# Optimization experiments

Measured on AMD Instinct MI355X. Metric: run time of the kernel, lower is better.

## Reference

```python
import jax, jax.numpy as jnp
import numpy as np

N, E, F_IN, HID, H, NG = 50000, 800000, 128, 64, 3, 50

def gatv2_layer(x, src, dst, Wsrc, bsrc, Wdst, bdst, attn, n_nodes):
    # DGL GATv2Conv: e_ij = attn . leaky_relu(Wsrc x_j + Wdst x_i), softmax over dst, aggregate Wsrc x_j
    Hh, O = attn.shape
    fs = (x @ Wsrc + bsrc).reshape(-1, Hh, O)  # [N,H,O]
    fd = (x @ Wdst + bdst).reshape(-1, Hh, O)
    e = jax.nn.leaky_relu(fs[src] + fd[dst], 0.2)          # [E,H,O]
    logits = jnp.einsum('eho,ho->eh', e, attn)             # [E,H]
    m = jax.ops.segment_max(logits, dst, num_segments=n_nodes)
    m = jnp.where(jnp.isfinite(m), m, 0.0)
    ex = jnp.exp(logits - m[dst])
    den = jax.ops.segment_sum(ex, dst, num_segments=n_nodes)
    alpha = ex / jnp.maximum(den[dst], 1e-9)               # edge softmax
    return jax.ops.segment_sum(alpha[..., None] * fs[src], dst, num_segments=n_nodes)  # [N,H,O]

def setup_inputs() -> dict:
    key = jax.random.key(0)
    ks = jax.random.split(key, 32)
    d = {}
    d['x'] = jax.random.normal(ks[0], (N, F_IN), jnp.float32)
    d['src'] = jax.random.randint(ks[1], (E,), 0, N)
    d['dst'] = jax.random.randint(ks[2], (E,), 0, N)
    d['graph_ids'] = jnp.sort(jax.random.randint(ks[3], (N,), 0, NG))
    d['n_graphs'] = NG
    ins = [F_IN, HID * H, HID * H]
    i = 4
    for l, fin in enumerate(ins, 1):
        s = 1.0 / np.sqrt(fin)
        d[f'Wsrc{l}'] = jax.random.normal(ks[i], (fin, H * HID), jnp.float32) * s; i += 1
        d[f'bsrc{l}'] = jnp.zeros((H * HID,), jnp.float32)
        d[f'Wdst{l}'] = jax.random.normal(ks[i], (fin, H * HID), jnp.float32) * s; i += 1
        d[f'bdst{l}'] = jnp.zeros((H * HID,), jnp.float32)
        d[f'attn{l}'] = jax.random.normal(ks[i], (H, HID), jnp.float32) * s; i += 1
    for name, (a, b) in [('1', (HID, 64)), ('2', (64, 32)), ('3', (32, 2))]:
        s = 1.0 / np.sqrt(a)
        d[f'W{name}'] = jax.random.normal(ks[i], (a, b), jnp.float32) * s; i += 1
        d[f'b{name}'] = jnp.zeros((b,), jnp.float32)
    return d

def forward(x, src, dst, graph_ids, n_graphs,
            Wsrc1, bsrc1, Wdst1, bdst1, attn1,
            Wsrc2, bsrc2, Wdst2, bdst2, attn2,
            Wsrc3, bsrc3, Wdst3, bdst3, attn3,
            W1, b1, W2, b2, W3, b3):
    n = x.shape[0]
    h = gatv2_layer(x, src, dst, Wsrc1, bsrc1, Wdst1, bdst1, attn1, n).reshape(n, -1)
    h = gatv2_layer(h, src, dst, Wsrc2, bsrc2, Wdst2, bdst2, attn2, n).reshape(n, -1)
    h = gatv2_layer(h, src, dst, Wsrc3, bsrc3, Wdst3, bdst3, attn3, n).mean(axis=1)  # [N,HID]
    # dgl.mean_nodes: per-graph mean pooling
    sums = jax.ops.segment_sum(h, graph_ids, num_segments=n_graphs)
    cnts = jax.ops.segment_sum(jnp.ones((n,), h.dtype), graph_ids, num_segments=n_graphs)
    g = sums / jnp.maximum(cnts, 1.0)[:, None]  # [NG,HID]
    lrelu = lambda t: jax.nn.leaky_relu(t, 0.01)
    out = lrelu(g @ W1 + b1)
    out = lrelu(out @ W2 + b2)
    out = lrelu(out @ W3 + b3)
    return out

def reference(x, src, dst, graph_ids, n_graphs,
              Wsrc1, bsrc1, Wdst1, bdst1, attn1,
              Wsrc2, bsrc2, Wdst2, bdst2, attn2,
              Wsrc3, bsrc3, Wdst3, bdst3, attn3,
              W1, b1, W2, b2, W3, b3):
    return forward(x, src, dst, graph_ids, n_graphs,
                   Wsrc1, bsrc1, Wdst1, bdst1, attn1,
                   Wsrc2, bsrc2, Wdst2, bdst2, attn2,
                   Wsrc3, bsrc3, Wdst3, bdst3, attn3,
                   W1, b1, W2, b2, W3, b3)
```

## Files before the change

kernel.cpp:

```cpp
#include <hip/hip_runtime.h>
#include <math.h>

#define N_NODES 50000
#define N_EDGES 800000
#define F_INPUT 128
#define HID 64
#define NHEAD 3
#define NGRAPH 50
#define D1 192
#define D2 384
#define NF 24
#define MF 3125

typedef __attribute__((ext_vector_type(8))) short bf16x8;
typedef __attribute__((ext_vector_type(4))) short short4v;
typedef __attribute__((ext_vector_type(4))) float f32x4;

#define ROR_ADD(v, C) \
  ((v) + __int_as_float(__builtin_amdgcn_update_dpp(0, __float_as_int(v), (C), 0xF, 0xF, true)))

__device__ __forceinline__ unsigned short f2bf(float x) {
  unsigned u = __float_as_uint(x);
  return (unsigned short)((u + 0x7FFFu + ((u >> 16) & 1u)) >> 16);
}
__device__ __forceinline__ float bf2f(unsigned short h) {
  return __uint_as_float(((unsigned)h) << 16);
}
__device__ __forceinline__ void split3(float x, unsigned short& o1, unsigned short& o2, unsigned short& o3) {
  o1 = f2bf(x); float f1 = bf2f(o1);
  float r1 = x - f1; o2 = f2bf(r1); float f2 = bf2f(o2);
  o3 = f2bf(r1 - f2);
}


__global__ void zero_int_kernel(int* __restrict__ p, int n) {
  int i = blockIdx.x * blockDim.x + threadIdx.x;
  if (i < n) p[i] = 0;
}

__global__ void hist_kernel(const int* __restrict__ dst, int* __restrict__ counts, int e) {
  int i = blockIdx.x * blockDim.x + threadIdx.x;
  if (i < e) atomicAdd(&counts[dst[i]], 1);
}

__global__ __launch_bounds__(256)
void scan_blocks_kernel(const int* __restrict__ counts, int* __restrict__ indptr,
                        int* __restrict__ bsum, int n) {
  __shared__ int wt[4];
  int tid = threadIdx.x, lane = tid & 63, wid = tid >> 6;
  int i = blockIdx.x * 256 + tid;
  int x = (i < n) ? counts[i] : 0;
  #pragma unroll
  for (int off = 1; off < 64; off <<= 1) {
    int t = __shfl_up(x, off, 64);
    if (lane >= off) x += t;
  }
  if (lane == 63) wt[wid] = x;
  __syncthreads();
  int woff = 0;
  #pragma unroll
  for (int w = 0; w < 4; ++w) if (w < wid) woff += wt[w];
  x += woff;
  if (i < n) indptr[i + 1] = x;
  if (tid == 255) bsum[blockIdx.x] = x;
}

__global__ __launch_bounds__(256)
void scan_sums_kernel(int* __restrict__ bsum, int nb) {
  __shared__ int wt[4];
  int tid = threadIdx.x, lane = tid & 63, wid = tid >> 6;
  int v = (tid < nb) ? bsum[tid] : 0;
  int x = v;
  #pragma unroll
  for (int off = 1; off < 64; off <<= 1) {
    int t = __shfl_up(x, off, 64);
    if (lane >= off) x += t;
  }
  if (lane == 63) wt[wid] = x;
  __syncthreads();
  int woff = 0;
  #pragma unroll
  for (int w = 0; w < 4; ++w) if (w < wid) woff += wt[w];
  if (tid < nb) bsum[tid] = woff + x - v;
}

__global__ void add_offs_kernel(int* __restrict__ indptr, const int* __restrict__ bsum,
                                int* __restrict__ cursor, int n) {
  int i = blockIdx.x * 256 + threadIdx.x;
  if (i == 0) { indptr[0] = 0; cursor[0] = 0; }
  if (i < n) {
    int v = indptr[i + 1] + bsum[blockIdx.x];
    indptr[i + 1] = v;
    if (i + 1 < n) cursor[i + 1] = v;
  }
}

__global__ void scatter_kernel(const int* __restrict__ src, const int* __restrict__ dst,
                               int* __restrict__ cursor, int* __restrict__ ssrc, int e) {
  int i = blockIdx.x * blockDim.x + threadIdx.x;
  if (i < e) {
    int pos = atomicAdd(&cursor[dst[i]], 1);
    ssrc[pos] = src[i];
  }
}


__global__ __launch_bounds__(256)
void wconv_kernel(const float* __restrict__ Wsrc, const float* __restrict__ Wdst,
                  const float* __restrict__ bsrc, const float* __restrict__ bdst,
                  int K, unsigned short* __restrict__ wfrag, float* __restrict__ biasf) {
  int t = blockIdx.x * 256 + threadIdx.x;
  if (t < D2) biasf[t] = (t < D1) ? bsrc[t] : bdst[t - D1];
  int KS = K >> 5;
  int total = KS * NF * 3 * 64;
  if (t >= total) return;
  int lane = t & 63;
  int q = t >> 6;
  int pl = q % 3; q /= 3;
  int nf = q % NF;
  int ks = q / NF;
  int n = nf * 16 + (lane & 15);
  int kg = lane >> 4;
  unsigned short out[8];
  #pragma unroll
  for (int j = 0; j < 8; ++j) {
    int k = ks * 32 + kg * 4 + (j & 3) + ((j >> 2) << 4);
    float w = (n < D1) ? Wsrc[(size_t)k * D1 + n] : Wdst[(size_t)k * D1 + (n - D1)];
    unsigned short s1, s2, s3;
    split3(w, s1, s2, s3);
    out[j] = (pl == 0) ? s1 : (pl == 1) ? s2 : s3;
  }
  *(bf16x8*)(wfrag + (size_t)t * 8) = *(bf16x8*)out;
}


__global__ __launch_bounds__(256)
void aconv_kernel(const float* __restrict__ A, unsigned short* __restrict__ P,
                  int n4, size_t MK) {
  int t = blockIdx.x * 256 + threadIdx.x;
  if (t >= n4) return;
  float4 v = ((const float4*)A)[t];
  unsigned short s1[4], s2[4], s3[4];
  split3(v.x, s1[0], s2[0], s3[0]);
  split3(v.y, s1[1], s2[1], s3[1]);
  split3(v.z, s1[2], s2[2], s3[2]);
  split3(v.w, s1[3], s2[3], s3[3]);
  ((short4v*)P)[t]        = *(short4v*)s1;
  ((short4v*)(P + MK))[t] = *(short4v*)s2;
  ((short4v*)(P + 2 * MK))[t] = *(short4v*)s3;
}


__global__ __launch_bounds__(256, 2)
void mfma_gemm_kernel(const unsigned short* __restrict__ Ap,
                      const unsigned short* __restrict__ Wf,
                      const float* __restrict__ biasf,
                      int K, float* __restrict__ C) {
  __shared__ unsigned short Bs[NF * 3 * 64 * 8];
  const int tid = threadIdx.x;
  const int lane = tid & 63, wid = tid >> 6;
  const int mf = blockIdx.x * 4 + wid;
  const bool active = (mf < MF);
  const int rowl = lane & 15;
  const int kg = lane >> 4;
  const size_t MK = (size_t)N_NODES * K;
  const int KS = K >> 5;

  f32x4 acc[NF];
  #pragma unroll
  for (int nf = 0; nf < NF; ++nf) acc[nf] = (f32x4){0.f, 0.f, 0.f, 0.f};

  const size_t arow = (size_t)(mf * 16 + rowl) * K;

  for (int ks = 0; ks < KS; ++ks) {
    {
      const float4* s = (const float4*)(Wf + (size_t)ks * (NF * 3 * 64 * 8));
      float4* d = (float4*)Bs;
      #pragma unroll
      for (int i = 0; i < 18; ++i) d[tid + i * 256] = s[tid + i * 256];
    }
    __syncthreads();
    if (active) {
      union { bf16x8 v; short4v h[2]; } ua1, ua2, ua3;
      const unsigned short* a0 = Ap + arow + ks * 32 + kg * 4;
      ua1.h[0] = *(const short4v*)(a0);
      ua1.h[1] = *(const short4v*)(a0 + 16);
      ua2.h[0] = *(const short4v*)(a0 + MK);
      ua2.h[1] = *(const short4v*)(a0 + MK + 16);
      ua3.h[0] = *(const short4v*)(a0 + 2 * MK);
      ua3.h[1] = *(const short4v*)(a0 + 2 * MK + 16);
      bf16x8 a1 = ua1.v, a2 = ua2.v, a3 = ua3.v;
      #pragma unroll
      for (int nf = 0; nf < NF; ++nf) {
        bf16x8 b1 = *(const bf16x8*)&Bs[(nf * 3 + 0) * 512 + lane * 8];
        bf16x8 b2 = *(const bf16x8*)&Bs[(nf * 3 + 1) * 512 + lane * 8];
        bf16x8 b3 = *(const bf16x8*)&Bs[(nf * 3 + 2) * 512 + lane * 8];
        acc[nf] = __builtin_amdgcn_mfma_f32_16x16x32_bf16(a1, b1, acc[nf], 0, 0, 0);
        acc[nf] = __builtin_amdgcn_mfma_f32_16x16x32_bf16(a1, b2, acc[nf], 0, 0, 0);
        acc[nf] = __builtin_amdgcn_mfma_f32_16x16x32_bf16(a2, b1, acc[nf], 0, 0, 0);
        acc[nf] = __builtin_amdgcn_mfma_f32_16x16x32_bf16(a1, b3, acc[nf], 0, 0, 0);
        acc[nf] = __builtin_amdgcn_mfma_f32_16x16x32_bf16(a2, b2, acc[nf], 0, 0, 0);
        acc[nf] = __builtin_amdgcn_mfma_f32_16x16x32_bf16(a3, b1, acc[nf], 0, 0, 0);
      }
    }
    __syncthreads();
  }

  if (active) {
    const int rowb = mf * 16 + kg * 4;
    #pragma unroll
    for (int nf = 0; nf < NF; ++nf) {
      int col = nf * 16 + rowl;
      float bb = biasf[col];
      float* cp = C + (size_t)rowb * D2 + col;
      cp[0]        = acc[nf][0] + bb;
      cp[D2]       = acc[nf][1] + bb;
      cp[2 * D2]   = acc[nf][2] + bb;
      cp[3 * D2]   = acc[nf][3] + bb;
    }
  }
}


template <int LAST>
__global__ __launch_bounds__(256)
void edge_kernel(const float* __restrict__ fsfd, const int* __restrict__ indptr,
                 const int* __restrict__ ssrc, const float* __restrict__ attn,
                 void* __restrict__ outv) {
  int wave = (blockIdx.x * blockDim.x + threadIdx.x) >> 6;
  if (wave >= N_NODES) return;
  int lane = threadIdx.x & 63;
  int grp = lane >> 4;
  int l16 = lane & 15;
  int db = l16 * 4;
  const int node = wave;
  const float LOG2E = 1.4426950408889634f;

  float fd[12], a[12];
  {
    const float* fdp = fsfd + (size_t)node * D2 + D1;
    *(float4*)&fd[0] = *(const float4*)(fdp + db);
    *(float4*)&fd[4] = *(const float4*)(fdp + 64 + db);
    *(float4*)&fd[8] = *(const float4*)(fdp + 128 + db);
    float4 a0 = *(const float4*)(attn + db);
    float4 a1 = *(const float4*)(attn + 64 + db);
    float4 a2 = *(const float4*)(attn + 128 + db);
    a[0]=a0.x*LOG2E; a[1]=a0.y*LOG2E; a[2]=a0.z*LOG2E; a[3]=a0.w*LOG2E;
    a[4]=a1.x*LOG2E; a[5]=a1.y*LOG2E; a[6]=a1.z*LOG2E; a[7]=a1.w*LOG2E;
    a[8]=a2.x*LOG2E; a[9]=a2.y*LOG2E; a[10]=a2.z*LOG2E; a[11]=a2.w*LOG2E;
  }
  int beg = indptr[node], end = indptr[node + 1];
  int deg = end - beg;
  int nit = (deg + 3) >> 2;

  float m[3] = {-INFINITY, -INFINITY, -INFINITY};
  float d[3] = {0.f, 0.f, 0.f};
  float c[12] = {0,0,0,0,0,0,0,0,0,0,0,0};
  float f[12] = {0,0,0,0,0,0,0,0,0,0,0,0};
  float g[12] = {0,0,0,0,0,0,0,0,0,0,0,0};

  int e0 = beg + grp;
  if (e0 < end) {
    int s = ssrc[e0];
    const float* p = fsfd + (size_t)s * D2;
    *(float4*)&f[0] = *(const float4*)(p + db);
    *(float4*)&f[4] = *(const float4*)(p + 64 + db);
    *(float4*)&f[8] = *(const float4*)(p + 128 + db);
  }
  int sNext = 0;
  { int e1 = e0 + 4; if (e1 < end) sNext = ssrc[e1]; }

  for (int it = 0; it < nit; ++it) {
    int eC = e0 + it * 4;
    int eN = eC + 4;
    int sNN = 0;
    { int e2 = eC + 8; if (e2 < end) sNN = ssrc[e2]; }
    if (eN < end) {
      const float* p = fsfd + (size_t)sNext * D2;
      *(float4*)&g[0] = *(const float4*)(p + db);
      *(float4*)&g[4] = *(const float4*)(p + 64 + db);
      *(float4*)&g[8] = *(const float4*)(p + 128 + db);
    }
    float ph0 = 0.f, ph1 = 0.f, ph2 = 0.f;
    #pragma unroll
    for (int i = 0; i < 4; ++i) {
      float t = f[i] + fd[i]; t = fmaxf(t, 0.2f * t); ph0 = fmaf(t, a[i], ph0);
    }
    #pragma unroll
    for (int i = 4; i < 8; ++i) {
      float t = f[i] + fd[i]; t = fmaxf(t, 0.2f * t); ph1 = fmaf(t, a[i], ph1);
    }
    #pragma unroll
    for (int i = 8; i < 12; ++i) {
      float t = f[i] + fd[i]; t = fmaxf(t, 0.2f * t); ph2 = fmaf(t, a[i], ph2);
    }
    ph0 = ROR_ADD(ph0, 0x128); ph1 = ROR_ADD(ph1, 0x128); ph2 = ROR_ADD(ph2, 0x128);
    ph0 = ROR_ADD(ph0, 0x124); ph1 = ROR_ADD(ph1, 0x124); ph2 = ROR_ADD(ph2, 0x124);
    ph0 = ROR_ADD(ph0, 0x122); ph1 = ROR_ADD(ph1, 0x122); ph2 = ROR_ADD(ph2, 0x122);
    ph0 = ROR_ADD(ph0, 0x121); ph1 = ROR_ADD(ph1, 0x121); ph2 = ROR_ADD(ph2, 0x121);
    if (eC < end) {
      {
        float nm = fmaxf(m[0], ph0);
        float ex = exp2f(-fabsf(ph0 - m[0]));
        float sc = (ph0 > m[0]) ? ex : 1.f;
        float p  = (ph0 > m[0]) ? 1.f : ex;
        d[0] = d[0] * sc + p; m[0] = nm;
        #pragma unroll
        for (int j = 0; j < 4; ++j) c[j] = fmaf(p, f[j], c[j] * sc);
      }
      {
        float nm = fmaxf(m[1], ph1);
        float ex = exp2f(-fabsf(ph1 - m[1]));
        float sc = (ph1 > m[1]) ? ex : 1.f;
        float p  = (ph1 > m[1]) ? 1.f : ex;
        d[1] = d[1] * sc + p; m[1] = nm;
        #pragma unroll
        for (int j = 0; j < 4; ++j) c[4 + j] = fmaf(p, f[4 + j], c[4 + j] * sc);
      }
      {
        float nm = fmaxf(m[2], ph2);
        float ex = exp2f(-fabsf(ph2 - m[2]));
        float sc = (ph2 > m[2]) ? ex : 1.f;
        float p  = (ph2 > m[2]) ? 1.f : ex;
        d[2] = d[2] * sc + p; m[2] = nm;
        #pragma unroll
        for (int j = 0; j < 4; ++j) c[8 + j] = fmaf(p, f[8 + j], c[8 + j] * sc);
      }
    }
    #pragma unroll
    for (int i = 0; i < 12; ++i) f[i] = g[i];
    sNext = sNN;
  }

  float M0 = m[0], M1 = m[1], M2 = m[2];
  #pragma unroll
  for (int off = 16; off < 64; off <<= 1) {
    M0 = fmaxf(M0, __shfl_xor(M0, off, 64));
    M1 = fmaxf(M1, __shfl_xor(M1, off, 64));
    M2 = fmaxf(M2, __shfl_xor(M2, off, 64));
  }
  float s0 = (m[0] == M0) ? 1.f : exp2f(m[0] - M0);
  float s1 = (m[1] == M1) ? 1.f : exp2f(m[1] - M1);
  float s2f = (m[2] == M2) ? 1.f : exp2f(m[2] - M2);
  d[0] *= s0; d[1] *= s1; d[2] *= s2f;
  #pragma unroll
  for (int j = 0; j < 4; ++j) { c[j] *= s0; c[4 + j] *= s1; c[8 + j] *= s2f; }
  #pragma unroll
  for (int off = 16; off < 64; off <<= 1) {
    d[0] += __shfl_xor(d[0], off, 64);
    d[1] += __shfl_xor(d[1], off, 64);
    d[2] += __shfl_xor(d[2], off, 64);
    #pragma unroll
    for (int i = 0; i < 12; ++i) c[i] += __shfl_xor(c[i], off, 64);
  }
  float r[12];
  float i0 = d[0] > 0.f ? 1.f / d[0] : 0.f;
  float i1 = d[1] > 0.f ? 1.f / d[1] : 0.f;
  float i2 = d[2] > 0.f ? 1.f / d[2] : 0.f;
  #pragma unroll
  for (int j = 0; j < 4; ++j) { r[j] = c[j] * i0; r[4 + j] = c[4 + j] * i1; r[8 + j] = c[8 + j] * i2; }

  if (grp == 0) {
    if (LAST) {
      float* out = (float*)outv;
      float4 o;
      o.x = (r[0] + r[4] + r[8])  * (1.f / 3.f);
      o.y = (r[1] + r[5] + r[9])  * (1.f / 3.f);
      o.z = (r[2] + r[6] + r[10]) * (1.f / 3.f);
      o.w = (r[3] + r[7] + r[11]) * (1.f / 3.f);
      *(float4*)(out + (size_t)node * HID + db) = o;
    } else {
      unsigned short* P = (unsigned short*)outv;
      const size_t MK2 = (size_t)N_NODES * D1;
      unsigned short s1[12], s2[12], s3[12];
      #pragma unroll
      for (int i = 0; i < 12; ++i) split3(r[i], s1[i], s2[i], s3[i]);
      #pragma unroll
      for (int hh = 0; hh < 3; ++hh) {
        size_t base = (size_t)node * D1 + hh * 64 + db;
        *(short4v*)(P + base)           = *(short4v*)&s1[hh * 4];
        *(short4v*)(P + MK2 + base)     = *(short4v*)&s2[hh * 4];
        *(short4v*)(P + 2 * MK2 + base) = *(short4v*)&s3[hh * 4];
      }
    }
  }
}


__global__ __launch_bounds__(256)
void pool_mlp_kernel(const float* __restrict__ h, const int* __restrict__ gids,
                     const float* __restrict__ W1, const float* __restrict__ b1,
                     const float* __restrict__ W2, const float* __restrict__ b2,
                     const float* __restrict__ W3, const float* __restrict__ b3,
                     float* __restrict__ out) {
  int g = blockIdx.x;
  int tid = threadIdx.x;
  int lane = tid & 63, wid = tid >> 6;
  int lo, hi;
  { int l = 0, r = N_NODES; while (l < r) { int mid = (l + r) >> 1; if (gids[mid] < g) l = mid + 1; else r = mid; } lo = l; }
  { int l = 0, r = N_NODES; while (l < r) { int mid = (l + r) >> 1; if (gids[mid] < g + 1) l = mid + 1; else r = mid; } hi = l; }
  float s = 0.f;
  for (int i = lo + wid; i < hi; i += 4) s += h[(size_t)i * HID + lane];
  __shared__ float red[4][64];
  __shared__ float gv[64], o1[64], o2[32];
  red[wid][lane] = s;
  __syncthreads();
  if (tid < 64) {
    float tot = red[0][tid] + red[1][tid] + red[2][tid] + red[3][tid];
    float cnt = (float)(hi - lo);
    gv[tid] = tot / fmaxf(cnt, 1.f);
  }
  __syncthreads();
  if (tid < 64) {
    float t = b1[tid];
    for (int k = 0; k < 64; ++k) t = fmaf(gv[k], W1[k * 64 + tid], t);
    o1[tid] = t > 0.f ? t : 0.01f * t;
  }
  __syncthreads();
  if (tid < 32) {
    float t = b2[tid];
    for (int k = 0; k < 64; ++k) t = fmaf(o1[k], W2[k * 32 + tid], t);
    o2[tid] = t > 0.f ? t : 0.01f * t;
  }
  __syncthreads();
  if (tid < 2) {
    float t = b3[tid];
    for (int k = 0; k < 32; ++k) t = fmaf(o2[k], W3[k * 2 + tid], t);
    out[g * 2 + tid] = t > 0.f ? t : 0.01f * t;
  }
}


extern "C" void kernel_launch(void* const* d_in, const int* in_sizes, int n_in,
                              void* d_out, int out_size, void* d_ws, size_t ws_size,
                              hipStream_t stream) {
  const float* x    = (const float*)d_in[0];
  const int*   src  = (const int*)d_in[1];
  const int*   dst  = (const int*)d_in[2];
  const int*   gids = (const int*)d_in[3];
  const float* Wsrc1 = (const float*)d_in[5];
  const float* bsrc1 = (const float*)d_in[6];
  const float* Wdst1 = (const float*)d_in[7];
  const float* bdst1 = (const float*)d_in[8];
  const float* attn1 = (const float*)d_in[9];
  const float* Wsrc2 = (const float*)d_in[10];
  const float* bsrc2 = (const float*)d_in[11];
  const float* Wdst2 = (const float*)d_in[12];
  const float* bdst2 = (const float*)d_in[13];
  const float* attn2 = (const float*)d_in[14];
  const float* Wsrc3 = (const float*)d_in[15];
  const float* bsrc3 = (const float*)d_in[16];
  const float* Wdst3 = (const float*)d_in[17];
  const float* bdst3 = (const float*)d_in[18];
  const float* attn3 = (const float*)d_in[19];
  const float* W1 = (const float*)d_in[20];
  const float* b1 = (const float*)d_in[21];
  const float* W2 = (const float*)d_in[22];
  const float* b2 = (const float*)d_in[23];
  const float* W3 = (const float*)d_in[24];
  const float* b3 = (const float*)d_in[25];
  float* out = (float*)d_out;

  float* fsfd = (float*)d_ws;
  unsigned short* planes = (unsigned short*)(fsfd + (size_t)N_NODES * D2);
  unsigned short* wfrag = planes + (size_t)3 * N_NODES * D1;
  float* biasf = (float*)(wfrag + 27648 * 8);
  int* counts  = (int*)(biasf + 384);
  int* indptr  = counts + N_NODES;
  int* ssrc    = indptr + (N_NODES + 1);
  int* bsum    = ssrc + N_EDGES;
  float* hlast = (float*)planes;

  const int NSCAN = (N_NODES + 255) / 256;

  zero_int_kernel<<<(N_NODES + 255) / 256, 256, 0, stream>>>(counts, N_NODES);
  hist_kernel<<<(N_EDGES + 255) / 256, 256, 0, stream>>>(dst, counts, N_EDGES);
  scan_blocks_kernel<<<NSCAN, 256, 0, stream>>>(counts, indptr, bsum, N_NODES);
  scan_sums_kernel<<<1, 256, 0, stream>>>(bsum, NSCAN);
  add_offs_kernel<<<NSCAN, 256, 0, stream>>>(indptr, bsum, counts, N_NODES);
  scatter_kernel<<<(N_EDGES + 255) / 256, 256, 0, stream>>>(src, dst, counts, ssrc, N_EDGES);

  dim3 egrid((N_NODES + 3) / 4);
  const int GG = (MF + 3) / 4;

  wconv_kernel<<<108, 256, 0, stream>>>(Wsrc1, Wdst1, bsrc1, bdst1, F_INPUT, wfrag, biasf);
  aconv_kernel<<<(N_NODES * F_INPUT / 4 + 255) / 256, 256, 0, stream>>>(
      x, planes, N_NODES * F_INPUT / 4, (size_t)N_NODES * F_INPUT);
  mfma_gemm_kernel<<<GG, 256, 0, stream>>>(planes, wfrag, biasf, F_INPUT, fsfd);
  edge_kernel<0><<<egrid, 256, 0, stream>>>(fsfd, indptr, ssrc, attn1, planes);

  wconv_kernel<<<108, 256, 0, stream>>>(Wsrc2, Wdst2, bsrc2, bdst2, D1, wfrag, biasf);
  mfma_gemm_kernel<<<GG, 256, 0, stream>>>(planes, wfrag, biasf, D1, fsfd);
  edge_kernel<0><<<egrid, 256, 0, stream>>>(fsfd, indptr, ssrc, attn2, planes);

  wconv_kernel<<<108, 256, 0, stream>>>(Wsrc3, Wdst3, bsrc3, bdst3, D1, wfrag, biasf);
  mfma_gemm_kernel<<<GG, 256, 0, stream>>>(planes, wfrag, biasf, D1, fsfd);
  edge_kernel<1><<<egrid, 256, 0, stream>>>(fsfd, indptr, ssrc, attn3, hlast);

  pool_mlp_kernel<<<NGRAPH, 256, 0, stream>>>(hlast, gids, W1, b1, W2, b2, W3, b3, out);
}
```

Before: 740.1 us.

## Store activation planes in MFMA fragment layout and retile GEMM across waves

The A operand (three bf16 split planes) is now written by aconv and the edge kernel directly in the MFMA fragment order, interleaved per 16-row tile and k-step, so the GEMM reads contiguous 16-byte fragments. The GEMM no longer stages all 24 weight fragments in shared memory behind barriers. Instead each wave covers 4 row tiles by 6 column tiles, reads B fragments straight from global memory, and reuses each B fragment across 4 row tiles. This removes the LDS staging and __syncthreads, trading them for more global/L2 B traffic and a scattered store pattern in the edge kernel.

Result: slower. 1.116 ms (+50.7%).

```diff
diff --git a/kernel.cpp b/kernel.cpp
--- a/kernel.cpp
+++ b/kernel.cpp
@@ -11,6 +11,7 @@
 #define D2 384
 #define NF 24
 #define MF 3125
+#define KS_L23 6
 
 typedef __attribute__((ext_vector_type(8))) short bf16x8;
 typedef __attribute__((ext_vector_type(4))) short short4v;
@@ -135,88 +136,88 @@
 
 
 __global__ __launch_bounds__(256)
-void aconv_kernel(const float* __restrict__ A, unsigned short* __restrict__ P,
-                  int n4, size_t MK) {
+void aconv_kernel(const float* __restrict__ A, unsigned short* __restrict__ Aq,
+                  int K, int KS) {
   int t = blockIdx.x * 256 + threadIdx.x;
-  if (t >= n4) return;
-  float4 v = ((const float4*)A)[t];
-  unsigned short s1[4], s2[4], s3[4];
-  split3(v.x, s1[0], s2[0], s3[0]);
-  split3(v.y, s1[1], s2[1], s3[1]);
-  split3(v.z, s1[2], s2[2], s3[2]);
-  split3(v.w, s1[3], s2[3], s3[3]);
-  ((short4v*)P)[t]        = *(short4v*)s1;
-  ((short4v*)(P + MK))[t] = *(short4v*)s2;
-  ((short4v*)(P + 2 * MK))[t] = *(short4v*)s3;
+  if (t >= MF * KS * 64) return;
+  int lane = t & 63;
+  int q = t >> 6;
+  int ks = q % KS;
+  int mf = q / KS;
+  int row = mf * 16 + (lane & 15);
+  int kg = lane >> 4;
+  const float* ap = A + (size_t)row * K + ks * 32 + kg * 4;
+  float4 v0 = *(const float4*)ap;
+  float4 v1 = *(const float4*)(ap + 16);
+  float vals[8] = {v0.x, v0.y, v0.z, v0.w, v1.x, v1.y, v1.z, v1.w};
+  unsigned short s1[8], s2[8], s3[8];
+  #pragma unroll
+  for (int j = 0; j < 8; ++j) split3(vals[j], s1[j], s2[j], s3[j]);
+  size_t base = (((size_t)mf * KS + ks) * 3) * 512 + lane * 8;
+  *(bf16x8*)(Aq + base)        = *(bf16x8*)s1;
+  *(bf16x8*)(Aq + base + 512)  = *(bf16x8*)s2;
+  *(bf16x8*)(Aq + base + 1024) = *(bf16x8*)s3;
 }
 
 
 __global__ __launch_bounds__(256, 2)
-void mfma_gemm_kernel(const unsigned short* __restrict__ Ap,
+void mfma_gemm_kernel(const unsigned short* __restrict__ Aq,
                       const unsigned short* __restrict__ Wf,
                       const float* __restrict__ biasf,
-                      int K, float* __restrict__ C) {
-  __shared__ unsigned short Bs[NF * 3 * 64 * 8];
-  const int tid = threadIdx.x;
-  const int lane = tid & 63, wid = tid >> 6;
-  const int mf = blockIdx.x * 4 + wid;
-  const bool active = (mf < MF);
-  const int rowl = lane & 15;
-  const int kg = lane >> 4;
-  const size_t MK = (size_t)N_NODES * K;
-  const int KS = K >> 5;
-
-  f32x4 acc[NF];
-  #pragma unroll
-  for (int nf = 0; nf < NF; ++nf) acc[nf] = (f32x4){0.f, 0.f, 0.f, 0.f};
-
-  const size_t arow = (size_t)(mf * 16 + rowl) * K;
+                      int KS, float* __restrict__ C) {
+  const int lane = threadIdx.x & 63;
+  const int w = threadIdx.x >> 6;
+  const int mfb = blockIdx.x * 4;
+  const int rowl = lane & 15, kg = lane >> 4;
+
+  f32x4 acc[4][6];
+  #pragma unroll
+  for (int mf = 0; mf < 4; ++mf)
+    #pragma unroll
+    for (int q = 0; q < 6; ++q) acc[mf][q] = (f32x4){0.f, 0.f, 0.f, 0.f};
 
   for (int ks = 0; ks < KS; ++ks) {
-    {
-      const float4* s = (const float4*)(Wf + (size_t)ks * (NF * 3 * 64 * 8));
-      float4* d = (float4*)Bs;
+    bf16x8 a[4][3];
+    #pragma unroll
+    for (int mf = 0; mf < 4; ++mf) {
+      int mfi = mfb + mf; if (mfi >= MF) mfi = MF - 1;
+      const unsigned short* ap = Aq + (((size_t)mfi * KS + ks) * 3) * 512 + lane * 8;
       #pragma unroll
-      for (int i = 0; i < 18; ++i) d[tid + i * 256] = s[tid + i * 256];
-    }
-    __syncthreads();
-    if (active) {
-      union { bf16x8 v; short4v h[2]; } ua1, ua2, ua3;
-      const unsigned short* a0 = Ap + arow + ks * 32 + kg * 4;
-      ua1.h[0] = *(const short4v*)(a0);
-      ua1.h[1] = *(const short4v*)(a0 + 16);
-      ua2.h[0] = *(const short4v*)(a0 + MK);
-      ua2.h[1] = *(const short4v*)(a0 + MK + 16);
-      ua3.h[0] = *(const short4v*)(a0 + 2 * MK);
-      ua3.h[1] = *(const short4v*)(a0 + 2 * MK + 16);
-      bf16x8 a1 = ua1.v, a2 = ua2.v, a3 = ua3.v;
+      for (int pl = 0; pl < 3; ++pl) a[mf][pl] = *(const bf16x8*)(ap + pl * 512);
+    }
+    #pragma unroll 2
+    for (int q = 0; q < 6; ++q) {
+      int nf = w * 6 + q;
+      const unsigned short* bp = Wf + ((size_t)(ks * NF + nf) * 3) * 512 + lane * 8;
+      bf16x8 b1 = *(const bf16x8*)(bp);
+      bf16x8 b2 = *(const bf16x8*)(bp + 512);
+      bf16x8 b3 = *(const bf16x8*)(bp + 1024);
       #pragma unroll
-      for (int nf = 0; nf < NF; ++nf) {
-        bf16x8 b1 = *(const bf16x8*)&Bs[(nf * 3 + 0) * 512 + lane * 8];
-        bf16x8 b2 = *(const bf16x8*)&Bs[(nf * 3 + 1) * 512 + lane * 8];
-        bf16x8 b3 = *(const bf16x8*)&Bs[(nf * 3 + 2) * 512 + lane * 8];
-        acc[nf] = __builtin_amdgcn_mfma_f32_16x16x32_bf16(a1, b1, acc[nf], 0, 0, 0);
-        acc[nf] = __builtin_amdgcn_mfma_f32_16x16x32_bf16(a1, b2, acc[nf], 0, 0, 0);
-        acc[nf] = __builtin_amdgcn_mfma_f32_16x16x32_bf16(a2, b1, acc[nf], 0, 0, 0);
-        acc[nf] = __builtin_amdgcn_mfma_f32_16x16x32_bf16(a1, b3, acc[nf], 0, 0, 0);
-        acc[nf] = __builtin_amdgcn_mfma_f32_16x16x32_bf16(a2, b2, acc[nf], 0, 0, 0);
-        acc[nf] = __builtin_amdgcn_mfma_f32_16x16x32_bf16(a3, b1, acc[nf], 0, 0, 0);
+      for (int mf = 0; mf < 4; ++mf) {
+        acc[mf][q] = __builtin_amdgcn_mfma_f32_16x16x32_bf16(a[mf][0], b1, acc[mf][q], 0, 0, 0);
+        acc[mf][q] = __builtin_amdgcn_mfma_f32_16x16x32_bf16(a[mf][0], b2, acc[mf][q], 0, 0, 0);
+        acc[mf][q] = __builtin_amdgcn_mfma_f32_16x16x32_bf16(a[mf][1], b1, acc[mf][q], 0, 0, 0);
+        acc[mf][q] = __builtin_amdgcn_mfma_f32_16x16x32_bf16(a[mf][0], b3, acc[mf][q], 0, 0, 0);
+        acc[mf][q] = __builtin_amdgcn_mfma_f32_16x16x32_bf16(a[mf][1], b2, acc[mf][q], 0, 0, 0);
+        acc[mf][q] = __builtin_amdgcn_mfma_f32_16x16x32_bf16(a[mf][2], b1, acc[mf][q], 0, 0, 0);
       }
     }
-    __syncthreads();
-  }
-
-  if (active) {
-    const int rowb = mf * 16 + kg * 4;
-    #pragma unroll
-    for (int nf = 0; nf < NF; ++nf) {
-      int col = nf * 16 + rowl;
+  }
+
+  #pragma unroll
+  for (int mf = 0; mf < 4; ++mf) {
+    int mfi = mfb + mf;
+    if (mfi >= MF) continue;
+    int rowb = mfi * 16 + kg * 4;
+    #pragma unroll
+    for (int q = 0; q < 6; ++q) {
+      int col = (w * 6 + q) * 16 + rowl;
       float bb = biasf[col];
       float* cp = C + (size_t)rowb * D2 + col;
-      cp[0]        = acc[nf][0] + bb;
-      cp[D2]       = acc[nf][1] + bb;
-      cp[2 * D2]   = acc[nf][2] + bb;
-      cp[3 * D2]   = acc[nf][3] + bb;
+      cp[0]      = acc[mf][q][0] + bb;
+      cp[D2]     = acc[mf][q][1] + bb;
+      cp[2 * D2] = acc[mf][q][2] + bb;
+      cp[3 * D2] = acc[mf][q][3] + bb;
     }
   }
 }
@@ -371,16 +372,22 @@
       *(float4*)(out + (size_t)node * HID + db) = o;
     } else {
       unsigned short* P = (unsigned short*)outv;
-      const size_t MK2 = (size_t)N_NODES * D1;
+      int mf = node >> 4, rl = node & 15;
       unsigned short s1[12], s2[12], s3[12];
       #pragma unroll
       for (int i = 0; i < 12; ++i) split3(r[i], s1[i], s2[i], s3[i]);
       #pragma unroll
       for (int hh = 0; hh < 3; ++hh) {
-        size_t base = (size_t)node * D1 + hh * 64 + db;
-        *(short4v*)(P + base)           = *(short4v*)&s1[hh * 4];
-        *(short4v*)(P + MK2 + base)     = *(short4v*)&s2[hh * 4];
-        *(short4v*)(P + 2 * MK2 + base) = *(short4v*)&s3[hh * 4];
+        int f0 = hh * 64 + db;
+        int ks = f0 >> 5;
+        int w32 = f0 & 31;
+        int kgx = (w32 & 15) >> 2;
+        int j0 = 4 * (w32 >> 4);
+        int ln = kgx * 16 + rl;
+        size_t base = (((size_t)mf * KS_L23 + ks) * 3) * 512 + ln * 8 + j0;
+        *(short4v*)(P + base)        = *(short4v*)&s1[hh * 4];
+        *(short4v*)(P + base + 512)  = *(short4v*)&s2[hh * 4];
+        *(short4v*)(P + base + 1024) = *(short4v*)&s3[hh * 4];
       }
     }
   }
@@ -484,17 +491,16 @@
   const int GG = (MF + 3) / 4;
 
   wconv_kernel<<<108, 256, 0, stream>>>(Wsrc1, Wdst1, bsrc1, bdst1, F_INPUT, wfrag, biasf);
-  aconv_kernel<<<(N_NODES * F_INPUT / 4 + 255) / 256, 256, 0, stream>>>(
-      x, planes, N_NODES * F_INPUT / 4, (size_t)N_NODES * F_INPUT);
-  mfma_gemm_kernel<<<GG, 256, 0, stream>>>(planes, wfrag, biasf, F_INPUT, fsfd);
+  aconv_kernel<<<(MF * 4 * 64 + 255) / 256, 256, 0, stream>>>(x, planes, F_INPUT, 4);
+  mfma_gemm_kernel<<<GG, 256, 0, stream>>>(planes, wfrag, biasf, 4, fsfd);
   edge_kernel<0><<<egrid, 256, 0, stream>>>(fsfd, indptr, ssrc, attn1, planes);
 
   wconv_kernel<<<108, 256, 0, stream>>>(Wsrc2, Wdst2, bsrc2, bdst2, D1, wfrag, biasf);
-  mfma_gemm_kernel<<<GG, 256, 0, stream>>>(planes, wfrag, biasf, D1, fsfd);
+  mfma_gemm_kernel<<<GG, 256, 0, stream>>>(planes, wfrag, biasf, 6, fsfd);
   edge_kernel<0><<<egrid, 256, 0, stream>>>(fsfd, indptr, ssrc, attn2, planes);
 
   wconv_kernel<<<108, 256, 0, stream>>>(Wsrc3, Wdst3, bsrc3, bdst3, D1, wfrag, biasf);
-  mfma_gemm_kernel<<<GG, 256, 0, stream>>>(planes, wfrag, biasf, D1, fsfd);
+  mfma_gemm_kernel<<<GG, 256, 0, stream>>>(planes, wfrag, biasf, 6, fsfd);
   edge_kernel<1><<<egrid, 256, 0, stream>>>(fsfd, indptr, ssrc, attn3, hlast);
 
   pool_mlp_kernel<<<NGRAPH, 256, 0, stream>>>(hlast, gids, W1, b1, W2, b2, W3, b3, out);
```
